# Kernel optimization log

Hardware: AMD Instinct MI355X
Metric: run time of the kernel (lower is better)

Reference implementation:

```python
import jax, jax.numpy as jnp
import numpy as np

MARGIN = 0.3
EPS = 1e-6  # torch pairwise_distance eps (added to the difference before norm)


def _sample_triplets(labels, B):
    """Vectorized equivalent of the per-row nonzero()+randint() mining loop.

    pos_idx[i] ~ Uniform{j : labels[j] == labels[i]}   (always non-empty: i itself)
    neg_idx[i] ~ Uniform{j : labels[j] != labels[i]}, fallback Uniform[0,B) if empty.
    Uniform-noise argmax over the masked set == uniform random choice.
    """
    key = jax.random.key(42)
    k1, k2, k3 = jax.random.split(key, 3)
    eq = labels[:, None] == labels[None, :]              # [B, B]
    pos_idx = jnp.argmax(jnp.where(eq, jax.random.uniform(k1, (B, B)), -1.0), axis=1)
    neg_scores = jnp.where(~eq, jax.random.uniform(k2, (B, B)), -1.0)
    has_neg = jnp.any(~eq, axis=1)
    neg_idx = jnp.where(has_neg,
                        jnp.argmax(neg_scores, axis=1),
                        jax.random.randint(k3, (B,), 0, B))
    return pos_idx, neg_idx


def _pdist(X, A, D):
    """out[i, j] = || A[j] - X[i] + EPS ||_2  (torch pairwise_distance semantics),
    computed via gram matrices instead of a [B,B,D] intermediate:
    ||a - x + eps||^2 = ||a||^2 + ||x||^2 - 2 a.x + 2*eps*(sum a - sum x) + D*eps^2.
    """
    sq = (jnp.sum(A * A, axis=1)[None, :]
          + jnp.sum(X * X, axis=1)[:, None]
          - 2.0 * (X @ A.T)
          + 2.0 * EPS * (jnp.sum(A, axis=1)[None, :] - jnp.sum(X, axis=1)[:, None])
          + D * EPS * EPS)
    return jnp.sqrt(jnp.maximum(sq, 1e-12))


def setup_inputs() -> dict:
    key = jax.random.key(0)
    kf, kl = jax.random.split(key)
    B, D, NUM_IDS = 4096, 1024, 512
    features = jax.random.normal(kf, (B, D), dtype=jnp.float32)
    labels = jax.random.randint(kl, (B,), 0, NUM_IDS, dtype=jnp.int32)
    return {"features": features, "labels": labels}


def reference(features, labels):
    B, D = features.shape
    pos_idx, neg_idx = _sample_triplets(labels, B)
    P = features[pos_idx]   # positives, [B, D]
    N = features[neg_idx]   # negatives, [B, D]
    # Original torch code stacks positives/negatives as [B,1,D] vs anchors [B,D],
    # so TripletMarginLoss broadcasts to ALL-PAIRS [B,B] distances:
    # dap[i, j] = ||anchor_j - positive_i + eps||, same for dan.
    dap = _pdist(P, features, D)  # [B, B]
    dan = _pdist(N, features, D)  # [B, B]
    return jnp.mean(jax.nn.relu(dap - dan + MARGIN))
```

## Files before the change

kernel.cpp:

```cpp
#include <hip/hip_runtime.h>
#include <stdint.h>

#define BSZ 4096
#define DIM 1024
#define EPSV 1e-6f
#define MARGINV 0.3f
#define LROWS 8

#define TF_ROT(x0, x1, r) { x0 += x1; x1 = ((x1 << r) | (x1 >> (32 - r))); x1 ^= x0; }

__host__ __device__ __forceinline__ void threefry2x32(uint32_t k0, uint32_t k1,
                                                      uint32_t c0, uint32_t c1,
                                                      uint32_t& o0, uint32_t& o1) {
  uint32_t ks2 = k0 ^ k1 ^ 0x1BD11BDAu;
  uint32_t x0 = c0 + k0;
  uint32_t x1 = c1 + k1;
  TF_ROT(x0, x1, 13) TF_ROT(x0, x1, 15) TF_ROT(x0, x1, 26) TF_ROT(x0, x1, 6)
  x0 += k1;  x1 += ks2 + 1u;
  TF_ROT(x0, x1, 17) TF_ROT(x0, x1, 29) TF_ROT(x0, x1, 16) TF_ROT(x0, x1, 24)
  x0 += ks2; x1 += k0 + 2u;
  TF_ROT(x0, x1, 13) TF_ROT(x0, x1, 15) TF_ROT(x0, x1, 26) TF_ROT(x0, x1, 6)
  x0 += k0;  x1 += k1 + 3u;
  TF_ROT(x0, x1, 17) TF_ROT(x0, x1, 29) TF_ROT(x0, x1, 16) TF_ROT(x0, x1, 24)
  x0 += k1;  x1 += ks2 + 4u;
  TF_ROT(x0, x1, 13) TF_ROT(x0, x1, 15) TF_ROT(x0, x1, 26) TF_ROT(x0, x1, 6)
  x0 += ks2; x1 += k0 + 5u;
  o0 = x0; o1 = x1;
}

__global__ __launch_bounds__(256) void prep_kernel(const float* __restrict__ F,
                                                   uint8_t* __restrict__ Fq,
                                                   float* __restrict__ norm2,
                                                   float* __restrict__ sums,
                                                   float* __restrict__ nv) {
  const int w = threadIdx.x >> 6, l = threadIdx.x & 63;
  const int r = blockIdx.x * 4 + w;
  const float4* src = (const float4*)(F + (size_t)r * DIM);
  uint32_t* dst = (uint32_t*)(Fq + (size_t)r * DIM);
  float s = 0.f, q = 0.f;
#pragma unroll
  for (int c = 0; c < 4; ++c) {
    float4 v = src[c * 64 + l];
    s += (v.x + v.y) + (v.z + v.w);
    q += v.x * v.x + v.y * v.y + v.z * v.z + v.w * v.w;
    int wd = 0;
    wd = __builtin_amdgcn_cvt_pk_fp8_f32(v.x, v.y, wd, false);
    wd = __builtin_amdgcn_cvt_pk_fp8_f32(v.z, v.w, wd, true);
    dst[c * 64 + l] = (uint32_t)wd;
  }
  for (int off = 32; off; off >>= 1) { s += __shfl_xor(s, off); q += __shfl_xor(q, off); }
  if (l == 0) {
    norm2[r] = q; sums[r] = s;
    nv[r] = q + 2.0f * EPSV * s;
  }
}

__global__ __launch_bounds__(256) void sample_kernel(const int* __restrict__ labels,
                                                     int* __restrict__ pos_idx,
                                                     int* __restrict__ neg_idx,
                                                     uint32_t p0, uint32_t p1,
                                                     uint32_t n0, uint32_t n1) {
  const int i = blockIdx.x, t = threadIdx.x;
  int lj[16];
#pragma unroll
  for (int c = 0; c < 16; ++c) lj[c] = labels[c * 256 + t];
  const int li = labels[i];
  const uint32_t base = (uint32_t)i * (uint32_t)BSZ + (uint32_t)t;
  const uint32_t nt = ~(uint32_t)t;

  unsigned long long bestn = 0ull;
#pragma unroll
  for (int c = 0; c < 16; ++c) {
    uint32_t y0, y1;
    threefry2x32(n0, n1, 0u, base + (uint32_t)(c * 256), y0, y1);
    const uint32_t mant = (y0 ^ y1) >> 9;
    const bool ne = (lj[c] != li);
    const uint32_t hi = ne ? mant : 0u;
    const uint32_t lo = ne ? (nt - (uint32_t)(c * 256)) : 0u;
    const unsigned long long key = ((unsigned long long)hi << 32) | lo;
    if (key > bestn) bestn = key;
  }

  unsigned long long bestp = 0ull;
#pragma unroll
  for (int c = 0; c < 16; ++c) {
    const bool eq = (lj[c] == li);
    if (__ballot(eq)) {
      uint32_t y0, y1;
      threefry2x32(p0, p1, 0u, base + (uint32_t)(c * 256), y0, y1);
      const uint32_t mant = (y0 ^ y1) >> 9;
      const uint32_t hi = eq ? mant : 0u;
      const uint32_t lo = eq ? (nt - (uint32_t)(c * 256)) : 0u;
      const unsigned long long key = ((unsigned long long)hi << 32) | lo;
      if (key > bestp) bestp = key;
    }
  }

  for (int off = 32; off; off >>= 1) {
    unsigned long long o;
    o = __shfl_xor(bestp, off); if (o > bestp) bestp = o;
    o = __shfl_xor(bestn, off); if (o > bestn) bestn = o;
  }
  __shared__ unsigned long long swp[4], swn[4];
  const int w = t >> 6, l = t & 63;
  if (l == 0) { swp[w] = bestp; swn[w] = bestn; }
  __syncthreads();
  if (t == 0) {
    unsigned long long vp = swp[0], vn = swn[0];
#pragma unroll
    for (int qd = 1; qd < 4; ++qd) {
      if (swp[qd] > vp) vp = swp[qd];
      if (swn[qd] > vn) vn = swn[qd];
    }
    pos_idx[i] = (int)(~(uint32_t)vp);
    neg_idx[i] = (vn == 0ull) ? 0 : (int)(~(uint32_t)vn);
  }
}

using int8v = __attribute__((ext_vector_type(8))) int;
using f32x4 = __attribute__((ext_vector_type(4))) float;

__device__ __forceinline__ void async_load16(const void* g, void* l) {
  __builtin_amdgcn_global_load_lds((__attribute__((address_space(1))) void*)g,
                                   (__attribute__((address_space(3))) void*)l, 16, 0, 0);
}

__global__ __launch_bounds__(256) void gemm_kernel(const uint8_t* __restrict__ Fq,
                                                   float* __restrict__ G) {
  const int p = blockIdx.x;
  int by = (int)((sqrtf(8.0f * (float)p + 1.0f) - 1.0f) * 0.5f);
  if ((by + 1) * (by + 2) / 2 <= p) ++by;
  if (by * (by + 1) / 2 > p) --by;
  const int bx = p - by * (by + 1) / 2;

  __shared__ __align__(16) uint8_t lA[128 * 128];
  __shared__ __align__(16) uint8_t lB[128 * 128];
  const int t = threadIdx.x;
  const int l = t & 63;
  const int w = t >> 6;
  const int wm = (w >> 1) * 64;
  const int wn = (w & 1) * 64;
  const int bm = bx * 128;
  const int bn = by * 128;

  f32x4 acc[4][4] = {};

  const int srow = t >> 3;
  const int scol = (t & 7) * 16;
  const uint8_t* gA0 = Fq + (size_t)(bm + srow) * DIM + scol;
  const uint8_t* gB0 = Fq + (size_t)(bn + srow) * DIM + scol;

  for (int it = 0; it < 8; ++it) {
    const int k0 = it * 128;
    __syncthreads();
#pragma unroll
    for (int ld = 0; ld < 4; ++ld) {
      async_load16(gA0 + (size_t)ld * 32 * DIM + k0, (char*)lA + (ld * 256 + t) * 16);
      async_load16(gB0 + (size_t)ld * 32 * DIM + k0, (char*)lB + (ld * 256 + t) * 16);
    }
    __syncthreads();
    const int fr = l & 15;
    const int fo = (l >> 4) * 32;
    int8v av[4], bv[4];
#pragma unroll
    for (int tm = 0; tm < 4; ++tm) av[tm] = *(const int8v*)&lA[(wm + tm * 16 + fr) * 128 + fo];
#pragma unroll
    for (int tn = 0; tn < 4; ++tn) bv[tn] = *(const int8v*)&lB[(wn + tn * 16 + fr) * 128 + fo];
#pragma unroll
    for (int tm = 0; tm < 4; ++tm)
#pragma unroll
      for (int tn = 0; tn < 4; ++tn)
        acc[tm][tn] = __builtin_amdgcn_mfma_scale_f32_16x16x128_f8f6f4(
            av[tm], bv[tn], acc[tm][tn],
            0, 0,
            0, 0x7F7F7F7F,
            0, 0x7F7F7F7F);
  }
  const int cr = (l >> 4) * 4;
  const int cc = l & 15;
#pragma unroll
  for (int tm = 0; tm < 4; ++tm)
#pragma unroll
    for (int tn = 0; tn < 4; ++tn) {
      const int row0 = bm + wm + tm * 16 + cr;
      const int col  = bn + wn + tn * 16 + cc;
#pragma unroll
      for (int r = 0; r < 4; ++r)
        G[(size_t)(row0 + r) * BSZ + col] = acc[tm][tn][r];
      float4 v = make_float4(acc[tm][tn][0], acc[tm][tn][1], acc[tm][tn][2], acc[tm][tn][3]);
      *(float4*)&G[(size_t)col * BSZ + row0] = v;
    }
}

__global__ __launch_bounds__(256) void loss_kernel(const float* __restrict__ G,
                                                   const float* __restrict__ norm2,
                                                   const float* __restrict__ sums,
                                                   const float* __restrict__ nv,
                                                   const int* __restrict__ pos_idx,
                                                   const int* __restrict__ neg_idx,
                                                   float* __restrict__ partial) {
  const int i0 = blockIdx.x * LROWS, t = threadIdx.x;
  const float deps2 = (float)DIM * EPSV * EPSV;
  float ca[LROWS], cb[LROWS];
  const float4* Ga[LROWS];
  const float4* Gb[LROWS];
#pragma unroll
  for (int r = 0; r < LROWS; ++r) {
    const int a = pos_idx[i0 + r], b = neg_idx[i0 + r];
    ca[r] = norm2[a] - 2.0f * EPSV * sums[a] + deps2;
    cb[r] = norm2[b] - 2.0f * EPSV * sums[b] + deps2;
    Ga[r] = (const float4*)(G + (size_t)a * BSZ);
    Gb[r] = (const float4*)(G + (size_t)b * BSZ);
  }
  const float4* N4 = (const float4*)nv;
  float s = 0.f;
#pragma unroll
  for (int c = 0; c < 4; ++c) {
    const int q = c * 256 + t;
    const float4 nj = N4[q];
#pragma unroll
    for (int r = 0; r < LROWS; ++r) {
      const float4 ga = Ga[r][q], gb = Gb[r][q];
      const float capr = ca[r], cbpr = cb[r];
      {
        const float dap = sqrtf(fmaxf(nj.x + capr - 2.f * ga.x, 1e-12f));
        const float dan = sqrtf(fmaxf(nj.x + cbpr - 2.f * gb.x, 1e-12f));
        s += fmaxf(dap - dan + MARGINV, 0.f);
      }
      {
        const float dap = sqrtf(fmaxf(nj.y + capr - 2.f * ga.y, 1e-12f));
        const float dan = sqrtf(fmaxf(nj.y + cbpr - 2.f * gb.y, 1e-12f));
        s += fmaxf(dap - dan + MARGINV, 0.f);
      }
      {
        const float dap = sqrtf(fmaxf(nj.z + capr - 2.f * ga.z, 1e-12f));
        const float dan = sqrtf(fmaxf(nj.z + cbpr - 2.f * gb.z, 1e-12f));
        s += fmaxf(dap - dan + MARGINV, 0.f);
      }
      {
        const float dap = sqrtf(fmaxf(nj.w + capr - 2.f * ga.w, 1e-12f));
        const float dan = sqrtf(fmaxf(nj.w + cbpr - 2.f * gb.w, 1e-12f));
        s += fmaxf(dap - dan + MARGINV, 0.f);
      }
    }
  }
  for (int off = 32; off; off >>= 1) s += __shfl_xor(s, off);
  __shared__ float ps[4];
  const int w = t >> 6, l = t & 63;
  if (l == 0) ps[w] = s;
  __syncthreads();
  if (t == 0) partial[blockIdx.x] = (ps[0] + ps[1]) + (ps[2] + ps[3]);
}

__global__ __launch_bounds__(256) void finalize_kernel(const float* __restrict__ partial,
                                                       float* __restrict__ out) {
  const int t = threadIdx.x;
  float s = partial[t] + partial[t + 256];
  for (int off = 32; off; off >>= 1) s += __shfl_xor(s, off);
  __shared__ float ps[4];
  const int w = t >> 6, l = t & 63;
  if (l == 0) ps[w] = s;
  __syncthreads();
  if (t == 0) out[0] = ((ps[0] + ps[1]) + (ps[2] + ps[3])) * (1.0f / ((float)BSZ * (float)BSZ));
}

extern "C" void kernel_launch(void* const* d_in, const int* in_sizes, int n_in,
                              void* d_out, int out_size, void* d_ws, size_t ws_size,
                              hipStream_t stream) {
  const float* feat = (const float*)d_in[0];
  const int* labels = (const int*)d_in[1];
  float* out = (float*)d_out;

  char* ws = (char*)d_ws;
  float* G        = (float*)ws;
  uint8_t* Fq     = (uint8_t*)(ws + (size_t)67108864);
  float* norm2    = (float*)(ws + (size_t)71303168);
  float* sums     = (float*)(ws + (size_t)71303168 + 16384);
  float* nv       = (float*)(ws + (size_t)71303168 + 32768);
  int* pos_idx    = (int*)  (ws + (size_t)71303168 + 49152);
  int* neg_idx    = (int*)  (ws + (size_t)71303168 + 65536);
  float* partial  = (float*)(ws + (size_t)71303168 + 81920);

  uint32_t k1a, k1b, k2a, k2b;
  threefry2x32(0u, 42u, 0u, 0u, k1a, k1b);
  threefry2x32(0u, 42u, 0u, 1u, k2a, k2b);

  prep_kernel<<<dim3(BSZ / 4), dim3(256), 0, stream>>>(feat, Fq, norm2, sums, nv);
  sample_kernel<<<dim3(BSZ), dim3(256), 0, stream>>>(labels, pos_idx, neg_idx, k1a, k1b, k2a, k2b);
  gemm_kernel<<<dim3(528), dim3(256), 0, stream>>>(Fq, G);
  loss_kernel<<<dim3(BSZ / LROWS), dim3(256), 0, stream>>>(G, norm2, sums, nv, pos_idx, neg_idx, partial);
  finalize_kernel<<<dim3(1), dim3(256), 0, stream>>>(partial, out);
}
```

Baseline: 163.0 us.

## Fuse triplet sampling into GEMM launch and fold finalize into loss kernel

Runs the sampling work as extra blocks inside the GEMM launch so the compute-bound GEMM and the RNG-heavy sampling share the GPU. Sampling now handles 8 rows per block and records positive candidates in a shared list, so the threefry hash for positives runs only on same-label entries. The finalize kernel is removed: loss blocks atomically add into an accumulator, and the last block (found via a ticket counter) writes the mean. Positive candidates are capped at 64 per row, and the float atomic sum makes the result order-dependent.

```diff
diff --git a/kernel.cpp b/kernel.cpp
--- a/kernel.cpp
+++ b/kernel.cpp
@@ -6,6 +6,9 @@
 #define EPSV 1e-6f
 #define MARGINV 0.3f
 #define LROWS 8
+#define GEMM_BLOCKS 528
+#define SROWS 8
+#define SAMPLE_BLOCKS (BSZ / SROWS)
 
 #define TF_ROT(x0, x1, r) { x0 += x1; x1 = ((x1 << r) | (x1 >> (32 - r))); x1 ^= x0; }
 
@@ -32,7 +35,9 @@
                                                    uint8_t* __restrict__ Fq,
                                                    float* __restrict__ norm2,
                                                    float* __restrict__ sums,
-                                                   float* __restrict__ nv) {
+                                                   float* __restrict__ nv,
+                                                   float* __restrict__ acc,
+                                                   unsigned int* __restrict__ ticket) {
   const int w = threadIdx.x >> 6, l = threadIdx.x & 63;
   const int r = blockIdx.x * 4 + w;
   const float4* src = (const float4*)(F + (size_t)r * DIM);
@@ -53,68 +58,7 @@
     norm2[r] = q; sums[r] = s;
     nv[r] = q + 2.0f * EPSV * s;
   }
-}
-
-__global__ __launch_bounds__(256) void sample_kernel(const int* __restrict__ labels,
-                                                     int* __restrict__ pos_idx,
-                                                     int* __restrict__ neg_idx,
-                                                     uint32_t p0, uint32_t p1,
-                                                     uint32_t n0, uint32_t n1) {
-  const int i = blockIdx.x, t = threadIdx.x;
-  int lj[16];
-#pragma unroll
-  for (int c = 0; c < 16; ++c) lj[c] = labels[c * 256 + t];
-  const int li = labels[i];
-  const uint32_t base = (uint32_t)i * (uint32_t)BSZ + (uint32_t)t;
-  const uint32_t nt = ~(uint32_t)t;
-
-  unsigned long long bestn = 0ull;
-#pragma unroll
-  for (int c = 0; c < 16; ++c) {
-    uint32_t y0, y1;
-    threefry2x32(n0, n1, 0u, base + (uint32_t)(c * 256), y0, y1);
-    const uint32_t mant = (y0 ^ y1) >> 9;
-    const bool ne = (lj[c] != li);
-    const uint32_t hi = ne ? mant : 0u;
-    const uint32_t lo = ne ? (nt - (uint32_t)(c * 256)) : 0u;
-    const unsigned long long key = ((unsigned long long)hi << 32) | lo;
-    if (key > bestn) bestn = key;
-  }
-
-  unsigned long long bestp = 0ull;
-#pragma unroll
-  for (int c = 0; c < 16; ++c) {
-    const bool eq = (lj[c] == li);
-    if (__ballot(eq)) {
-      uint32_t y0, y1;
-      threefry2x32(p0, p1, 0u, base + (uint32_t)(c * 256), y0, y1);
-      const uint32_t mant = (y0 ^ y1) >> 9;
-      const uint32_t hi = eq ? mant : 0u;
-      const uint32_t lo = eq ? (nt - (uint32_t)(c * 256)) : 0u;
-      const unsigned long long key = ((unsigned long long)hi << 32) | lo;
-      if (key > bestp) bestp = key;
-    }
-  }
-
-  for (int off = 32; off; off >>= 1) {
-    unsigned long long o;
-    o = __shfl_xor(bestp, off); if (o > bestp) bestp = o;
-    o = __shfl_xor(bestn, off); if (o > bestn) bestn = o;
-  }
-  __shared__ unsigned long long swp[4], swn[4];
-  const int w = t >> 6, l = t & 63;
-  if (l == 0) { swp[w] = bestp; swn[w] = bestn; }
-  __syncthreads();
-  if (t == 0) {
-    unsigned long long vp = swp[0], vn = swn[0];
-#pragma unroll
-    for (int qd = 1; qd < 4; ++qd) {
-      if (swp[qd] > vp) vp = swp[qd];
-      if (swn[qd] > vn) vn = swn[qd];
-    }
-    pos_idx[i] = (int)(~(uint32_t)vp);
-    neg_idx[i] = (vn == 0ull) ? 0 : (int)(~(uint32_t)vn);
-  }
+  if (blockIdx.x == 0 && threadIdx.x == 0) { acc[0] = 0.f; ticket[0] = 0u; }
 }
 
 using int8v = __attribute__((ext_vector_type(8))) int;
@@ -125,8 +69,72 @@
                                    (__attribute__((address_space(3))) void*)l, 16, 0, 0);
 }
 
-__global__ __launch_bounds__(256) void gemm_kernel(const uint8_t* __restrict__ Fq,
-                                                   float* __restrict__ G) {
+__global__ __launch_bounds__(256) void gemm_sample_kernel(const uint8_t* __restrict__ Fq,
+                                                          float* __restrict__ G,
+                                                          const int* __restrict__ labels,
+                                                          int* __restrict__ pos_idx,
+                                                          int* __restrict__ neg_idx,
+                                                          uint32_t p0, uint32_t p1,
+                                                          uint32_t n0, uint32_t n1) {
+  if (blockIdx.x >= GEMM_BLOCKS) {
+    __shared__ unsigned long long swp[SROWS], swn[SROWS];
+    __shared__ int plist[SROWS][64];
+    __shared__ int pcnt[SROWS];
+    const int t = threadIdx.x;
+    const int i0 = (blockIdx.x - GEMM_BLOCKS) * SROWS;
+    if (t < SROWS) { swp[t] = 0ull; swn[t] = 0ull; pcnt[t] = 0; }
+    int lj[16];
+#pragma unroll
+    for (int c = 0; c < 16; ++c) lj[c] = labels[c * 256 + t];
+    __syncthreads();
+    const uint32_t nt = ~(uint32_t)t;
+    const int lane = t & 63;
+    for (int r = 0; r < SROWS; ++r) {
+      const int li = labels[i0 + r];
+      const uint32_t base = (uint32_t)(i0 + r) * (uint32_t)BSZ + (uint32_t)t;
+      unsigned long long bestn = 0ull;
+#pragma unroll
+      for (int c = 0; c < 16; ++c) {
+        uint32_t y0, y1;
+        threefry2x32(n0, n1, 0u, base + (uint32_t)(c * 256), y0, y1);
+        const uint32_t mant = (y0 ^ y1) >> 9;
+        const bool eq = (lj[c] == li);
+        if (eq) {
+          int sl = atomicAdd(&pcnt[r], 1);
+          if (sl < 64) plist[r][sl] = c * 256 + t;
+        }
+        const uint32_t hi = eq ? 0u : mant;
+        const uint32_t lo = eq ? 0u : (nt - (uint32_t)(c * 256));
+        const unsigned long long key = ((unsigned long long)hi << 32) | lo;
+        if (key > bestn) bestn = key;
+      }
+      for (int off = 32; off; off >>= 1) {
+        unsigned long long o = __shfl_xor(bestn, off);
+        if (o > bestn) bestn = o;
+      }
+      if (lane == 0) atomicMax(&swn[r], bestn);
+    }
+    __syncthreads();
+    for (int r = 0; r < SROWS; ++r) {
+      const int cnt = pcnt[r] < 64 ? pcnt[r] : 64;
+      if (t < cnt) {
+        const int j = plist[r][t];
+        uint32_t y0, y1;
+        threefry2x32(p0, p1, 0u, (uint32_t)(i0 + r) * (uint32_t)BSZ + (uint32_t)j, y0, y1);
+        const uint32_t mant = (y0 ^ y1) >> 9;
+        const unsigned long long key =
+            ((unsigned long long)mant << 32) | (uint32_t)(~j);
+        atomicMax(&swp[r], key);
+      }
+    }
+    __syncthreads();
+    if (t < SROWS) {
+      pos_idx[i0 + t] = (int)(~(uint32_t)swp[t]);
+      const unsigned long long vn = swn[t];
+      neg_idx[i0 + t] = (vn == 0ull) ? 0 : (int)(~(uint32_t)vn);
+    }
+    return;
+  }
   const int p = blockIdx.x;
   int by = (int)((sqrtf(8.0f * (float)p + 1.0f) - 1.0f) * 0.5f);
   if ((by + 1) * (by + 2) / 2 <= p) ++by;
@@ -198,7 +206,9 @@
                                                    const float* __restrict__ nv,
                                                    const int* __restrict__ pos_idx,
                                                    const int* __restrict__ neg_idx,
-                                                   float* __restrict__ partial) {
+                                                   float* __restrict__ acc,
+                                                   unsigned int* __restrict__ ticket,
+                                                   float* __restrict__ out) {
   const int i0 = blockIdx.x * LROWS, t = threadIdx.x;
   const float deps2 = (float)DIM * EPSV * EPSV;
   float ca[LROWS], cb[LROWS];
@@ -249,19 +259,16 @@
   const int w = t >> 6, l = t & 63;
   if (l == 0) ps[w] = s;
   __syncthreads();
-  if (t == 0) partial[blockIdx.x] = (ps[0] + ps[1]) + (ps[2] + ps[3]);
-}
-
-__global__ __launch_bounds__(256) void finalize_kernel(const float* __restrict__ partial,
-                                                       float* __restrict__ out) {
-  const int t = threadIdx.x;
-  float s = partial[t] + partial[t + 256];
-  for (int off = 32; off; off >>= 1) s += __shfl_xor(s, off);
-  __shared__ float ps[4];
-  const int w = t >> 6, l = t & 63;
-  if (l == 0) ps[w] = s;
-  __syncthreads();
-  if (t == 0) out[0] = ((ps[0] + ps[1]) + (ps[2] + ps[3])) * (1.0f / ((float)BSZ * (float)BSZ));
+  if (t == 0) {
+    atomicAdd(acc, (ps[0] + ps[1]) + (ps[2] + ps[3]));
+    __threadfence();
+    unsigned int old = __hip_atomic_fetch_add(ticket, 1u, __ATOMIC_ACQ_REL,
+                                              __HIP_MEMORY_SCOPE_AGENT);
+    if (old == (unsigned int)(gridDim.x - 1)) {
+      float total = __hip_atomic_load(acc, __ATOMIC_ACQUIRE, __HIP_MEMORY_SCOPE_AGENT);
+      out[0] = total * (1.0f / ((float)BSZ * (float)BSZ));
+    }
+  }
 }
 
 extern "C" void kernel_launch(void* const* d_in, const int* in_sizes, int n_in,
@@ -272,22 +279,23 @@
   float* out = (float*)d_out;
 
   char* ws = (char*)d_ws;
-  float* G        = (float*)ws;
-  uint8_t* Fq     = (uint8_t*)(ws + (size_t)67108864);
-  float* norm2    = (float*)(ws + (size_t)71303168);
-  float* sums     = (float*)(ws + (size_t)71303168 + 16384);
-  float* nv       = (float*)(ws + (size_t)71303168 + 32768);
-  int* pos_idx    = (int*)  (ws + (size_t)71303168 + 49152);
-  int* neg_idx    = (int*)  (ws + (size_t)71303168 + 65536);
-  float* partial  = (float*)(ws + (size_t)71303168 + 81920);
+  float* G         = (float*)ws;
+  uint8_t* Fq      = (uint8_t*)(ws + (size_t)67108864);
+  float* norm2     = (float*)(ws + (size_t)71303168);
+  float* sums      = (float*)(ws + (size_t)71303168 + 16384);
+  float* nv        = (float*)(ws + (size_t)71303168 + 32768);
+  int* pos_idx     = (int*)  (ws + (size_t)71303168 + 49152);
+  int* neg_idx     = (int*)  (ws + (size_t)71303168 + 65536);
+  float* acc       = (float*)(ws + (size_t)71303168 + 81920);
+  unsigned int* tk = (unsigned int*)(ws + (size_t)71303168 + 81924);
 
   uint32_t k1a, k1b, k2a, k2b;
   threefry2x32(0u, 42u, 0u, 0u, k1a, k1b);
   threefry2x32(0u, 42u, 0u, 1u, k2a, k2b);
 
-  prep_kernel<<<dim3(BSZ / 4), dim3(256), 0, stream>>>(feat, Fq, norm2, sums, nv);
-  sample_kernel<<<dim3(BSZ), dim3(256), 0, stream>>>(labels, pos_idx, neg_idx, k1a, k1b, k2a, k2b);
-  gemm_kernel<<<dim3(528), dim3(256), 0, stream>>>(Fq, G);
-  loss_kernel<<<dim3(BSZ / LROWS), dim3(256), 0, stream>>>(G, norm2, sums, nv, pos_idx, neg_idx, partial);
-  finalize_kernel<<<dim3(1), dim3(256), 0, stream>>>(partial, out);
-}
+  prep_kernel<<<dim3(BSZ / 4), dim3(256), 0, stream>>>(feat, Fq, norm2, sums, nv, acc, tk);
+  gemm_sample_kernel<<<dim3(GEMM_BLOCKS + SAMPLE_BLOCKS), dim3(256), 0, stream>>>(
+      Fq, G, labels, pos_idx, neg_idx, k1a, k1b, k2a, k2b);
+  loss_kernel<<<dim3(BSZ / LROWS), dim3(256), 0, stream>>>(G, norm2, sums, nv, pos_idx,
+                                                           neg_idx, acc, tk, out);
+}
```

Result: slower. 184.9 us (+13.4%).
